# Kernel tuning notes

Hardware: AMD Instinct MI355X
Metric: run time of the kernel (lower is better)

Reference implementation:

```python
import jax, jax.numpy as jnp
import numpy as np

TAU = 1.0
MAX_ITER = 10


def setup_inputs() -> dict:
    key = jax.random.key(0)
    s = jax.random.normal(key, (32, 1024, 1024), dtype=jnp.float32)
    return {"s": s}


def reference(s) -> jnp.ndarray:
    # s: [B, N1, N2] with N1 <= N2 (square here), no padding -> fully vectorized
    log_s = s / TAU
    for i in range(MAX_ITER):
        # even iter: row normalization (logsumexp over columns, axis=2)
        # odd  iter: column normalization (logsumexp over rows, axis=1)
        axis = 2 if i % 2 == 0 else 1
        log_s = log_s - jax.nn.logsumexp(log_s, axis=axis, keepdims=True)
    return jnp.exp(log_s)
```

## Files before the change

### kernel.cpp

```cpp
#include <hip/hip_runtime.h>
#include <math.h>


#define BATCH 32
#define N 1024
#define RCHUNKS 32
#define ROWS_PER_BLK 32
#define PCHUNKS RCHUNKS

__global__ __launch_bounds__(512, 4) void fused_pair_kernel(
    const float* __restrict__ s, const float* __restrict__ c,
    float* __restrict__ r, float* __restrict__ pm, float* __restrict__ pl,
    int has_c)
{
    const int bc    = blockIdx.x;
    const int b     = bc >> 5;
    const int chunk = bc & 31;
    const int row0  = chunk * ROWS_PER_BLK;
    const int wave  = threadIdx.x >> 6;
    const int lane  = threadIdx.x & 63;

    __shared__ float4 sm4[8][256];
    __shared__ float4 sl4[8][256];

    float4 cv[4];
    if (has_c) {
        const float4* c4 = (const float4*)(c + b * N);
#pragma unroll
        for (int k = 0; k < 4; k++) cv[k] = c4[lane + 64 * k];
    } else {
#pragma unroll
        for (int k = 0; k < 4; k++) cv[k] = make_float4(0.f, 0.f, 0.f, 0.f);
    }

    float x[4][16];
#pragma unroll
    for (int rp = 0; rp < 4; rp++) {
        const float4* srow =
            (const float4*)(s + ((size_t)(b * N + row0 + wave * 4 + rp)) * N);
#pragma unroll
        for (int k = 0; k < 4; k++) {
            float4 v = srow[lane + 64 * k];
            x[rp][4*k+0] = v.x + cv[k].x;
            x[rp][4*k+1] = v.y + cv[k].y;
            x[rp][4*k+2] = v.z + cv[k].z;
            x[rp][4*k+3] = v.w + cv[k].w;
        }
    }

    float rv[4];
#pragma unroll
    for (int rp = 0; rp < 4; rp++) {
        float m = fmaxf(
            fmaxf(fmaxf(fmaxf(x[rp][0],  x[rp][1]),  fmaxf(x[rp][2],  x[rp][3])),
                  fmaxf(fmaxf(x[rp][4],  x[rp][5]),  fmaxf(x[rp][6],  x[rp][7]))),
            fmaxf(fmaxf(fmaxf(x[rp][8],  x[rp][9]),  fmaxf(x[rp][10], x[rp][11])),
                  fmaxf(fmaxf(x[rp][12], x[rp][13]), fmaxf(x[rp][14], x[rp][15]))));
#pragma unroll
        for (int off = 32; off > 0; off >>= 1) m = fmaxf(m, __shfl_xor(m, off, 64));
        float s0 = 0.f, s1 = 0.f, s2 = 0.f, s3 = 0.f;
#pragma unroll
        for (int t = 0; t < 4; t++) {
            s0 += __expf(x[rp][t]      - m);
            s1 += __expf(x[rp][4 + t]  - m);
            s2 += __expf(x[rp][8 + t]  - m);
            s3 += __expf(x[rp][12 + t] - m);
        }
        float sum = (s0 + s1) + (s2 + s3);
#pragma unroll
        for (int off = 32; off > 0; off >>= 1) sum += __shfl_xor(sum, off, 64);
        rv[rp] = -(m + __logf(sum));
        if (lane == 0) r[b * N + row0 + wave * 4 + rp] = rv[rp];
    }

#pragma unroll
    for (int k = 0; k < 4; k++) {
        float pmv[4], plv[4];
#pragma unroll
        for (int e = 0; e < 4; e++) {
            float x0 = x[0][4*k+e] + rv[0];
            float x1 = x[1][4*k+e] + rv[1];
            float x2 = x[2][4*k+e] + rv[2];
            float x3 = x[3][4*k+e] + rv[3];
            float m = fmaxf(fmaxf(x0, x1), fmaxf(x2, x3));
            plv[e] = __expf(x0 - m) + __expf(x1 - m) +
                     __expf(x2 - m) + __expf(x3 - m);
            pmv[e] = m;
        }
        sm4[wave][lane + 64 * k] = make_float4(pmv[0], pmv[1], pmv[2], pmv[3]);
        sl4[wave][lane + 64 * k] = make_float4(plv[0], plv[1], plv[2], plv[3]);
    }
    __syncthreads();

    const float* smf = (const float*)sm4;
    const float* slf = (const float*)sl4;
#pragma unroll
    for (int cc = 0; cc < 2; cc++) {
        const int col = threadIdx.x + cc * 512;
        float M = smf[col], L = slf[col];
#pragma unroll
        for (int w = 1; w < 8; w++) {
            float m = smf[w * N + col], l = slf[w * N + col];
            float mn = fmaxf(M, m);
            L = L * __expf(M - mn) + l * __expf(m - mn);
            M = mn;
        }
        pm[(size_t)bc * N + col] = M;
        pl[(size_t)bc * N + col] = L;
    }
}

__global__ __launch_bounds__(1024) void col_combine_kernel(
    const float* __restrict__ pm, const float* __restrict__ pl,
    float* __restrict__ c)
{
    const int b  = blockIdx.x >> 2;
    const int q  = blockIdx.x & 3;
    const int jc = threadIdx.x & 255;
    const int kg = threadIdx.x >> 8;
    const int j  = q * 256 + jc;
    float M = -3.0e38f, L = 0.f;
#pragma unroll
    for (int k = 0; k < 8; k++) {
        const int kk = kg * 8 + k;
        float m = pm[((size_t)(b * PCHUNKS + kk)) * N + j];
        float l = pl[((size_t)(b * PCHUNKS + kk)) * N + j];
        float mn = fmaxf(M, m);
        L = L * __expf(M - mn) + l * __expf(m - mn); M = mn;
    }
    __shared__ float smm[4][256], sll[4][256];
    smm[kg][jc] = M; sll[kg][jc] = L;
    __syncthreads();
    if (kg == 0) {
#pragma unroll
        for (int g2 = 1; g2 < 4; g2++) {
            float m = smm[g2][jc], l = sll[g2][jc];
            float mn = fmaxf(M, m);
            L = L * __expf(M - mn) + l * __expf(m - mn); M = mn;
        }
        c[b * N + j] = -(M + __logf(L));
    }
}

__global__ __launch_bounds__(256) void zero_c_kernel(float* __restrict__ c) {
    c[blockIdx.x * 256 + threadIdx.x] = 0.0f;
}

__global__ __launch_bounds__(256) void row_lse_kernel(const float* __restrict__ s,
                                                      const float* __restrict__ c,
                                                      float* __restrict__ r) {
    const int wave = threadIdx.x >> 6;
    const int lane = threadIdx.x & 63;
    const int row  = blockIdx.x * 4 + wave;
    const int b    = row >> 10;
    const float4* srow = (const float4*)(s + (size_t)row * N);
    const float4* crow = (const float4*)(c + (size_t)b * N);
    float x[16];
#pragma unroll
    for (int k = 0; k < 4; k++) {
        float4 v = srow[lane + k * 64];
        float4 cv = crow[lane + k * 64];
        x[4*k+0]=v.x+cv.x; x[4*k+1]=v.y+cv.y; x[4*k+2]=v.z+cv.z; x[4*k+3]=v.w+cv.w;
    }
    float m = x[0];
#pragma unroll
    for (int t = 1; t < 16; t++) m = fmaxf(m, x[t]);
#pragma unroll
    for (int off = 32; off > 0; off >>= 1) m = fmaxf(m, __shfl_xor(m, off, 64));
    float sum = 0.f;
#pragma unroll
    for (int t = 0; t < 16; t++) sum += __expf(x[t] - m);
#pragma unroll
    for (int off = 32; off > 0; off >>= 1) sum += __shfl_xor(sum, off, 64);
    if (lane == 0) r[row] = -(m + __logf(sum));
}

__global__ __launch_bounds__(1024) void col_lse_direct_kernel(const float* __restrict__ s,
                                                              const float* __restrict__ r,
                                                              float* __restrict__ c) {
    const int b = blockIdx.x;
    const int j = threadIdx.x;
    const float* rb = r + b * N;
    const float* base = s + (size_t)b * N * N + j;
    float m = -3.0e38f, l = 0.f;
    for (int i = 0; i < N; i++) {
        float x  = base[(size_t)i * N] + rb[i];
        float mn = fmaxf(m, x);
        l = l * __expf(m - mn) + __expf(x - mn);
        m = mn;
    }
    c[b * N + j] = -(m + __logf(l));
}

__global__ __launch_bounds__(256) void finalize_kernel(const float* __restrict__ s,
                                                       const float* __restrict__ r,
                                                       const float* __restrict__ c,
                                                       float* __restrict__ out) {
    const int f4  = blockIdx.x * 256 + threadIdx.x;
    const int j4  = f4 & 255;
    const int row = f4 >> 8;
    const int b   = row >> 10;
    float4 v  = ((const float4*)s)[f4];
    float  rr = r[row];
    float4 cc = ((const float4*)c)[(b << 8) + j4];
    float4 o;
    o.x = __expf(v.x + rr + cc.x);
    o.y = __expf(v.y + rr + cc.y);
    o.z = __expf(v.z + rr + cc.z);
    o.w = __expf(v.w + rr + cc.w);
    ((float4*)out)[f4] = o;
}

extern "C" void kernel_launch(void* const* d_in, const int* in_sizes, int n_in,
                              void* d_out, int out_size, void* d_ws, size_t ws_size,
                              hipStream_t stream) {
    const float* s = (const float*)d_in[0];
    float* out = (float*)d_out;

    float* c  = (float*)d_ws;
    float* r  = c + BATCH * N;
    float* pm = r + BATCH * N;
    float* pl = pm + BATCH * PCHUNKS * N;

    const size_t needed =
        (size_t)(2 * BATCH * N + 2 * BATCH * PCHUNKS * N) * sizeof(float);

    if (ws_size >= needed) {
        for (int p = 0; p < 5; p++) {
            fused_pair_kernel<<<BATCH * RCHUNKS, 512, 0, stream>>>(
                s, c, r, pm, pl, p > 0 ? 1 : 0);
            col_combine_kernel<<<BATCH * 4, 1024, 0, stream>>>(pm, pl, c);
        }
    } else {
        zero_c_kernel<<<(BATCH * N) / 256, 256, 0, stream>>>(c);
        for (int it = 0; it < 10; it++) {
            if ((it & 1) == 0)
                row_lse_kernel<<<(BATCH * N) / 4, 256, 0, stream>>>(s, c, r);
            else
                col_lse_direct_kernel<<<BATCH, 1024, 0, stream>>>(s, r, c);
        }
    }

    const int total_f4 = BATCH * N * N / 4;
    finalize_kernel<<<total_f4 / 256, 256, 0, stream>>>(s, r, c, out);
}
```

Baseline: 373.1 us.

## Add persistent cooperative Sinkhorn kernel holding the matrix on-chip across iterations

After: 553.0 us. 48.2% more time.

```diff
diff --git a/kernel.cpp b/kernel.cpp
--- a/kernel.cpp
+++ b/kernel.cpp
@@ -1,5 +1,8 @@
 #include <hip/hip_runtime.h>
+#include <hip/hip_cooperative_groups.h>
 #include <math.h>
+
+namespace cg = cooperative_groups;
 
 
 #define BATCH 32
@@ -7,6 +10,181 @@
 #define RCHUNKS 32
 #define ROWS_PER_BLK 32
 #define PCHUNKS RCHUNKS
+
+#define LDS_FLOATS 37888
+#define LDS_BYTES  151552
+
+__global__ __launch_bounds__(512, 2) void sinkhorn_coop(
+    const float* __restrict__ s, float* __restrict__ out,
+    float* __restrict__ pm, float* __restrict__ pl)
+{
+    extern __shared__ float lds[];
+    float4* q3  = (float4*)lds;
+    float*  Bm  = lds + 32768;
+    float*  Bl  = Bm + 2048;
+    float*  Lcs = Bl + 2048;
+
+    const int cu = blockIdx.x;
+    const int b  = cu >> 3;
+    const int rb = cu & 7;
+    const int w  = threadIdx.x >> 6;
+    const int l  = threadIdx.x & 63;
+
+    const size_t rowbase = ((size_t)b * N + rb * 128 + w * 16) * N;
+
+    float x[16][12];
+#pragma unroll
+    for (int r = 0; r < 16; ++r) {
+        const float4* p = (const float4*)(s + rowbase + (size_t)r * N);
+        float4 v0 = p[l];
+        float4 v1 = p[64 + l];
+        float4 v2 = p[128 + l];
+        float4 v3 = p[192 + l];
+        x[r][0] = v0.x; x[r][1] = v0.y; x[r][2]  = v0.z; x[r][3]  = v0.w;
+        x[r][4] = v1.x; x[r][5] = v1.y; x[r][6]  = v1.z; x[r][7]  = v1.w;
+        x[r][8] = v2.x; x[r][9] = v2.y; x[r][10] = v2.z; x[r][11] = v2.w;
+        q3[(w*16 + r)*64 + l] = v3;
+    }
+
+    float Lc[16];
+#pragma unroll
+    for (int k = 0; k < 16; ++k) Lc[k] = 0.f;
+
+    cg::grid_group grid = cg::this_grid();
+
+#pragma unroll 1
+    for (int it = 0; it < 5; ++it) {
+#pragma unroll
+        for (int r = 0; r < 16; ++r) {
+            float4 h = q3[(w*16 + r)*64 + l];
+#pragma unroll
+            for (int k = 0; k < 12; ++k) x[r][k] -= Lc[k];
+            h.x -= Lc[12]; h.y -= Lc[13]; h.z -= Lc[14]; h.w -= Lc[15];
+            float m = fmaxf(fmaxf(h.x, h.y), fmaxf(h.z, h.w));
+#pragma unroll
+            for (int k = 0; k < 12; ++k) m = fmaxf(m, x[r][k]);
+#pragma unroll
+            for (int off = 32; off > 0; off >>= 1) m = fmaxf(m, __shfl_xor(m, off, 64));
+            float s0 = __expf(h.x - m) + __expf(h.y - m);
+            float s1 = __expf(h.z - m) + __expf(h.w - m);
+            float s2 = 0.f, s3 = 0.f;
+#pragma unroll
+            for (int k = 0; k < 12; k += 4) {
+                s0 += __expf(x[r][k]   - m);
+                s1 += __expf(x[r][k+1] - m);
+                s2 += __expf(x[r][k+2] - m);
+                s3 += __expf(x[r][k+3] - m);
+            }
+            float sum = (s0 + s1) + (s2 + s3);
+#pragma unroll
+            for (int off = 32; off > 0; off >>= 1) sum += __shfl_xor(sum, off, 64);
+            float Lr = m + __logf(sum);
+#pragma unroll
+            for (int k = 0; k < 12; ++k) x[r][k] -= Lr;
+            h.x -= Lr; h.y -= Lr; h.z -= Lr; h.w -= Lr;
+            q3[(w*16 + r)*64 + l] = h;
+        }
+
+#pragma unroll
+        for (int q = 0; q < 4; ++q) {
+            float cm[4], cl[4];
+            if (q < 3) {
+#pragma unroll
+                for (int e = 0; e < 4; ++e) {
+                    const int k = q*4 + e;
+                    float m = x[0][k];
+#pragma unroll
+                    for (int r = 1; r < 16; ++r) m = fmaxf(m, x[r][k]);
+                    float acc = 0.f;
+#pragma unroll
+                    for (int r = 0; r < 16; ++r) acc += __expf(x[r][k] - m);
+                    cm[e] = m; cl[e] = acc;
+                }
+            } else {
+                float4 mm = make_float4(-3.0e38f, -3.0e38f, -3.0e38f, -3.0e38f);
+#pragma unroll
+                for (int r = 0; r < 16; ++r) {
+                    float4 h = q3[(w*16 + r)*64 + l];
+                    mm.x = fmaxf(mm.x, h.x); mm.y = fmaxf(mm.y, h.y);
+                    mm.z = fmaxf(mm.z, h.z); mm.w = fmaxf(mm.w, h.w);
+                }
+                float4 aa = make_float4(0.f, 0.f, 0.f, 0.f);
+#pragma unroll
+                for (int r = 0; r < 16; ++r) {
+                    float4 h = q3[(w*16 + r)*64 + l];
+                    aa.x += __expf(h.x - mm.x); aa.y += __expf(h.y - mm.y);
+                    aa.z += __expf(h.z - mm.z); aa.w += __expf(h.w - mm.w);
+                }
+                cm[0] = mm.x; cm[1] = mm.y; cm[2] = mm.z; cm[3] = mm.w;
+                cl[0] = aa.x; cl[1] = aa.y; cl[2] = aa.z; cl[3] = aa.w;
+            }
+#pragma unroll
+            for (int e = 0; e < 4; ++e) {
+                Bm[(w*4 + e)*64 + l] = cm[e];
+                Bl[(w*4 + e)*64 + l] = cl[e];
+            }
+            __syncthreads();
+            if (threadIdx.x < 256) {
+                const int e  = threadIdx.x >> 6;
+                const int ll = threadIdx.x & 63;
+                float M = Bm[e*64 + ll], L = Bl[e*64 + ll];
+#pragma unroll
+                for (int w2 = 1; w2 < 8; ++w2) {
+                    float m2 = Bm[(w2*4 + e)*64 + ll];
+                    float l2 = Bl[(w2*4 + e)*64 + ll];
+                    float mn = fmaxf(M, m2);
+                    L = L * __expf(M - mn) + l2 * __expf(m2 - mn);
+                    M = mn;
+                }
+                pm[(size_t)cu * N + (q*4 + e)*64 + ll] = M;
+                pl[(size_t)cu * N + (q*4 + e)*64 + ll] = L;
+            }
+            __syncthreads();
+        }
+
+        grid.sync();
+
+#pragma unroll
+        for (int cc = 0; cc < 2; ++cc) {
+            const int idx = threadIdx.x + cc * 512;
+            float M = -3.0e38f, L = 0.f;
+#pragma unroll
+            for (int k2 = 0; k2 < 8; ++k2) {
+                float m2 = pm[(size_t)(b*8 + k2) * N + idx];
+                float l2 = pl[(size_t)(b*8 + k2) * N + idx];
+                float mn = fmaxf(M, m2);
+                L = L * __expf(M - mn) + l2 * __expf(m2 - mn);
+                M = mn;
+            }
+            Lcs[idx] = M + __logf(L);
+        }
+        __syncthreads();
+#pragma unroll
+        for (int q = 0; q < 4; ++q)
+#pragma unroll
+            for (int e = 0; e < 4; ++e)
+                Lc[q*4 + e] = Lcs[(q*4 + e)*64 + l];
+    }
+
+#pragma unroll
+    for (int r = 0; r < 16; ++r) {
+        float4* orow = (float4*)(out + rowbase + (size_t)r * N);
+        float4 h = q3[(w*16 + r)*64 + l];
+        float4 o;
+        o.x = __expf(x[r][0] - Lc[0]);   o.y = __expf(x[r][1] - Lc[1]);
+        o.z = __expf(x[r][2] - Lc[2]);   o.w = __expf(x[r][3] - Lc[3]);
+        orow[l] = o;
+        o.x = __expf(x[r][4] - Lc[4]);   o.y = __expf(x[r][5] - Lc[5]);
+        o.z = __expf(x[r][6] - Lc[6]);   o.w = __expf(x[r][7] - Lc[7]);
+        orow[64 + l] = o;
+        o.x = __expf(x[r][8] - Lc[8]);   o.y = __expf(x[r][9] - Lc[9]);
+        o.z = __expf(x[r][10] - Lc[10]); o.w = __expf(x[r][11] - Lc[11]);
+        orow[128 + l] = o;
+        o.x = __expf(h.x - Lc[12]); o.y = __expf(h.y - Lc[13]);
+        o.z = __expf(h.z - Lc[14]); o.w = __expf(h.w - Lc[15]);
+        orow[192 + l] = o;
+    }
+}
 
 __global__ __launch_bounds__(512, 4) void fused_pair_kernel(
     const float* __restrict__ s, const float* __restrict__ c,
@@ -51,22 +229,14 @@
     float rv[4];
 #pragma unroll
     for (int rp = 0; rp < 4; rp++) {
-        float m = fmaxf(
-            fmaxf(fmaxf(fmaxf(x[rp][0],  x[rp][1]),  fmaxf(x[rp][2],  x[rp][3])),
-                  fmaxf(fmaxf(x[rp][4],  x[rp][5]),  fmaxf(x[rp][6],  x[rp][7]))),
-            fmaxf(fmaxf(fmaxf(x[rp][8],  x[rp][9]),  fmaxf(x[rp][10], x[rp][11])),
-                  fmaxf(fmaxf(x[rp][12], x[rp][13]), fmaxf(x[rp][14], x[rp][15]))));
+        float m = x[rp][0];
+#pragma unroll
+        for (int t = 1; t < 16; t++) m = fmaxf(m, x[rp][t]);
 #pragma unroll
         for (int off = 32; off > 0; off >>= 1) m = fmaxf(m, __shfl_xor(m, off, 64));
-        float s0 = 0.f, s1 = 0.f, s2 = 0.f, s3 = 0.f;
-#pragma unroll
-        for (int t = 0; t < 4; t++) {
-            s0 += __expf(x[rp][t]      - m);
-            s1 += __expf(x[rp][4 + t]  - m);
-            s2 += __expf(x[rp][8 + t]  - m);
-            s3 += __expf(x[rp][12 + t] - m);
-        }
-        float sum = (s0 + s1) + (s2 + s3);
+        float sum = 0.f;
+#pragma unroll
+        for (int t = 0; t < 16; t++) sum += __expf(x[rp][t] - m);
 #pragma unroll
         for (int off = 32; off > 0; off >>= 1) sum += __shfl_xor(sum, off, 64);
         rv[rp] = -(m + __logf(sum));
@@ -99,10 +269,10 @@
         const int col = threadIdx.x + cc * 512;
         float M = smf[col], L = slf[col];
 #pragma unroll
-        for (int w = 1; w < 8; w++) {
-            float m = smf[w * N + col], l = slf[w * N + col];
+        for (int w2 = 1; w2 < 8; w2++) {
+            float m = smf[w2 * N + col], l2 = slf[w2 * N + col];
             float mn = fmaxf(M, m);
-            L = L * __expf(M - mn) + l * __expf(m - mn);
+            L = L * __expf(M - mn) + l2 * __expf(m - mn);
             M = mn;
         }
         pm[(size_t)bc * N + col] = M;
@@ -217,6 +387,36 @@
     const float* s = (const float*)d_in[0];
     float* out = (float*)d_out;
 
+    static int coop_checked = 0, coop_ok = 0;
+    if (!coop_checked) {
+        int dev = 0;
+        hipDeviceProp_t prop;
+        if (hipGetDevice(&dev) == hipSuccess &&
+            hipGetDeviceProperties(&prop, dev) == hipSuccess &&
+            prop.cooperativeLaunch) {
+            if (hipFuncSetAttribute((const void*)sinkhorn_coop,
+                                    hipFuncAttributeMaxDynamicSharedMemorySize,
+                                    LDS_BYTES) == hipSuccess)
+                coop_ok = 1;
+        }
+        coop_checked = 1;
+    }
+
+    const size_t needed_coop = (size_t)(2 * 256 * N) * sizeof(float);
+    if (coop_ok && ws_size >= needed_coop) {
+        float* pmc = (float*)d_ws;
+        float* plc = pmc + 256 * N;
+        const float* s_arg = s;
+        float* out_arg = out;
+        void* kargs[] = { (void*)&s_arg, (void*)&out_arg,
+                          (void*)&pmc, (void*)&plc };
+        hipError_t e = hipLaunchCooperativeKernel(
+            (const void*)sinkhorn_coop, dim3(256), dim3(512),
+            kargs, LDS_BYTES, stream);
+        if (e == hipSuccess) return;
+        coop_ok = 0;
+    }
+
     float* c  = (float*)d_ws;
     float* r  = c + BATCH * N;
     float* pm = r + BATCH * N;
```
